# Performance work log

Hardware: AMD Instinct MI355X
Metric: run time of the kernel (lower is better)

The kernel has to match this reference:

```python
import jax, jax.numpy as jnp
import numpy as np

B, D, K, A = 32768, 256, 1024, 32
MIN_LOG_STD, MAX_LOG_STD = -20.0, 2.0


def setup_inputs() -> dict:
    key = jax.random.key(0)
    ks = jax.random.split(key, 9)
    return {
        "obs": jax.random.normal(ks[0], (B, D), dtype=jnp.float32),
        "mean_C": jax.random.normal(ks[1], (K, D), dtype=jnp.float32),
        "mean_sigma": jnp.abs(jax.random.normal(ks[2], (K,), dtype=jnp.float32)) + 0.1,
        "mean_w": jax.random.normal(ks[3], (A, K), dtype=jnp.float32),
        "mean_b": jax.random.normal(ks[4], (A,), dtype=jnp.float32),
        "std_C": jax.random.normal(ks[5], (K, D), dtype=jnp.float32),
        "std_sigma": jnp.abs(jax.random.normal(ks[6], (K,), dtype=jnp.float32)) + 0.1,
        "std_w": jax.random.normal(ks[7], (A, K), dtype=jnp.float32),
        "std_b": jax.random.normal(ks[8], (A,), dtype=jnp.float32),
    }


def _rbf(x, C, sigma_sq, w, b):
    # r[b,k] = sum_d (x[b,d] - C[k,d])^2, expanded to avoid a [B,K,D] intermediate
    x2 = jnp.sum(x * x, axis=-1, keepdims=True)           # [B,1]
    c2 = jnp.sum(C * C, axis=-1)[None, :]                  # [1,K]
    r = x2 - 2.0 * (x @ C.T) + c2                          # [B,K]
    phi = jnp.exp(-r / (2.0 * jnp.abs(sigma_sq)[None, :]))  # [B,K]
    return phi @ w.T + b[None, :]                          # [B,A]


def reference(obs, mean_C, mean_sigma, mean_w, mean_b,
              std_C, std_sigma, std_w, std_b):
    action_mean = _rbf(obs, mean_C, mean_sigma, mean_w, mean_b)
    std_raw = _rbf(obs, std_C, std_sigma, std_w, std_b)
    action_std = jnp.exp(jnp.clip(std_raw, MIN_LOG_STD, MAX_LOG_STD))
    return jnp.concatenate((action_mean, action_std), axis=-1)  # [B, 2A]
```

## Files before the change

kernel.cpp:

```cpp
#include <hip/hip_runtime.h>


typedef float floatx4 __attribute__((ext_vector_type(4)));
typedef int   intx4  __attribute__((ext_vector_type(4)));
typedef unsigned int u32;
typedef unsigned char u8;

constexpr float LOG2E = 1.4426950408889634f;
constexpr float QS    = 25.4f;
constexpr float SINV2 = (5.0f / 127.0f) * (5.0f / 127.0f);

__device__ __forceinline__ u32 pk_fp8(float a, float b, float c, float d) {
  u32 v = __builtin_amdgcn_cvt_pk_fp8_f32(a, b, 0u, 0);
  v = __builtin_amdgcn_cvt_pk_fp8_f32(c, d, v, 1);
  return v;
}
__device__ __forceinline__ long mk64(u32 lo, u32 hi) {
  return (long)lo | ((long)hi << 32);
}
__device__ __forceinline__ int q8(float x) {
  return (int)rintf(fminf(fmaxf(x * QS, -127.f), 127.f));
}
__device__ __forceinline__ u32 pk_i8(int a, int b, int c, int d) {
  return (u32)(a & 255) | ((u32)(b & 255) << 8) | ((u32)(c & 255) << 16) | ((u32)(d & 255) << 24);
}

__global__ void prep(const float* __restrict__ mC, const float* __restrict__ mS,
                     const float* __restrict__ sC, const float* __restrict__ sS,
                     const float* __restrict__ mw, const float* __restrict__ sw,
                     u8* __restrict__ Cb2, float* __restrict__ a2g,
                     float* __restrict__ g2n, u8* __restrict__ wt)
{
  const int blk = blockIdx.x;
  if (blk < 512) {
    const int wq = threadIdx.x >> 6;
    const int t  = threadIdx.x & 63;
    const int b  = blk * 4 + wq;
    const int half = b >> 10;
    const int k = b & 1023;
    const float* src = (half ? sC : mC) + (size_t)k * 256;
    float4 f = *(const float4*)(src + t * 4);
    int i0 = q8(f.x), i1 = q8(f.y), i2 = q8(f.z), i3 = q8(f.w);
    const int ct = b >> 6, row = b & 63;
    const int wvv = row >> 4, cc = row & 15;
    const int ks = t >> 4, qq = (t >> 2) & 3, j0 = (t & 3) * 4;
    *(u32*)(Cb2 + (size_t)ct * 16384 + wvv * 4096 + (ks * 64 + qq * 16 + cc) * 16 + j0) =
        pk_i8(i0, i1, i2, i3);
    int is = i0 * i0 + i1 * i1 + i2 * i2 + i3 * i3;
    for (int off = 32; off > 0; off >>= 1) is += __shfl_down(is, off, 64);
    if (t == 0) {
      float sig = fabsf((half ? sS : mS)[k]);
      float t2 = SINV2 * LOG2E * 0.5f / sig;
      a2g[b] = 2.f * t2;
      g2n[b] = -t2 * (float)is;
    }
  } else {
    const int m   = blk - 512;
    const int tid = threadIdx.x;
    const int wv  = tid >> 6;
    const int lane = tid & 63;
    const int c   = lane & 15;
    const int q   = lane >> 4;
    const int kbE = ((2 * m) & 15) * 64 + 16 * wv + 4 * q;
    const float* src = (m < 8) ? mw : sw;
    float4 f00 = *(const float4*)(src + (size_t)c * 1024 + kbE);
    float4 f01 = *(const float4*)(src + (size_t)c * 1024 + kbE + 64);
    float4 f10 = *(const float4*)(src + (size_t)(16 + c) * 1024 + kbE);
    float4 f11 = *(const float4*)(src + (size_t)(16 + c) * 1024 + kbE + 64);
    uint4 o;
    o.x = pk_fp8(f00.x, f00.y, f00.z, f00.w);
    o.y = pk_fp8(f01.x, f01.y, f01.z, f01.w);
    o.z = pk_fp8(f10.x, f10.y, f10.z, f10.w);
    o.w = pk_fp8(f11.x, f11.y, f11.z, f11.w);
    *(uint4*)(wt + ((size_t)m * 256 + tid) * 16) = o;
  }
}

__global__ __launch_bounds__(256, 4)
void policy_main(const float* __restrict__ obs,
                 const u8* __restrict__ Cb2,
                 const float* __restrict__ a2g,
                 const float* __restrict__ g2n,
                 const u8* __restrict__ wt,
                 const float* __restrict__ mbias,
                 const float* __restrict__ sbias,
                 float* __restrict__ out)
{
  __shared__ __align__(16) char smem[18432];
  float* x2p = (float*)(smem + 8192);
  float* red = (float*)smem;

  const int tid  = threadIdx.x;
  const int lane = tid & 63;
  const int wv   = tid >> 6;
  const int c    = lane & 15;
  const int q    = lane >> 4;
  const int half = blockIdx.x & 1;
  const int row0 = (blockIdx.x >> 1) * 32;
  const int kslc = 16 * wv + 4 * q;
  const int cfo  = wv * 4096 + lane * 16;

  const u8*    cbh = Cb2 + (size_t)half * (16 * 16384);
  const float* a2h = a2g + half * 1024;
  const float* g2h = g2n + half * 1024;
  const u8*    wtl = wt + (size_t)half * 32768 + (size_t)tid * 16;

#define LOADCF(CF, t)                                                     \
  { const u8* g0_ = cbh + (size_t)(t) * 16384 + cfo;                      \
    CF[0] = *(const intx4*)(g0_);                                         \
    CF[1] = *(const intx4*)(g0_ + 1024);                                  \
    CF[2] = *(const intx4*)(g0_ + 2048);                                  \
    CF[3] = *(const intx4*)(g0_ + 3072); }

  intx4 cfU[4], cfV[4];
  LOADCF(cfU, 0)
  LOADCF(cfV, 1)

  #pragma unroll
  for (int i = 0; i < 2; ++i) {
    int s = i * 256 + tid;
    int row = s >> 4;
    int s16 = s & 15;
    int l16 = s16 ^ (row & 15);
    const float* src = obs + (size_t)(row0 + row) * 256 + l16 * 16;
    float4 f0 = ((const float4*)src)[0];
    float4 f1 = ((const float4*)src)[1];
    float4 f2 = ((const float4*)src)[2];
    float4 f3 = ((const float4*)src)[3];
    int a0 = q8(f0.x), a1v = q8(f0.y), a2v = q8(f0.z), a3 = q8(f0.w);
    int b0 = q8(f1.x), b1 = q8(f1.y), b2 = q8(f1.z), b3 = q8(f1.w);
    int c0 = q8(f2.x), c1 = q8(f2.y), c2 = q8(f2.z), c3 = q8(f2.w);
    int d0 = q8(f3.x), d1 = q8(f3.y), d2 = q8(f3.z), d3 = q8(f3.w);
    uint4 pk;
    pk.x = pk_i8(a0, a1v, a2v, a3);
    pk.y = pk_i8(b0, b1, b2, b3);
    pk.z = pk_i8(c0, c1, c2, c3);
    pk.w = pk_i8(d0, d1, d2, d3);
    *(uint4*)(smem + s * 16) = pk;
    int is = a0*a0 + a1v*a1v + a2v*a2v + a3*a3
           + b0*b0 + b1*b1 + b2*b2 + b3*b3
           + c0*c0 + c1*c1 + c2*c2 + c3*c3
           + d0*d0 + d1*d1 + d2*d2 + d3*d3;
    x2p[row * 16 + s16] = (float)is;
  }
  __syncthreads();

  intx4 ob[2][4];
  #pragma unroll
  for (int nt = 0; nt < 2; ++nt) {
    const int row = nt * 16 + c;
    #pragma unroll
    for (int ks = 0; ks < 4; ++ks) {
      int slot = (4 * ks + q) ^ (row & 15);
      ob[nt][ks] = *(const intx4*)(smem + row * 256 + slot * 16);
    }
  }
  if (tid < 32) {
    float ssum = 0.f;
    #pragma unroll
    for (int j = 0; j < 16; j += 4) {
      float4 a = *(const float4*)(x2p + tid * 16 + j);
      ssum += a.x + a.y + a.z + a.w;
    }
    x2p[512 + tid] = ssum;
  }
  __syncthreads();

  float hx2[2];
  hx2[0] = 0.5f * x2p[512 + c];
  hx2[1] = 0.5f * x2p[512 + 16 + c];

  const intx4 Z4i = {0, 0, 0, 0};
  const floatx4 Z4 = {0.f, 0.f, 0.f, 0.f};
  floatx4 acc[2][2];
  #pragma unroll
  for (int a2i = 0; a2i < 2; ++a2i)
    #pragma unroll
    for (int nt = 0; nt < 2; ++nt) acc[a2i][nt] = Z4;

  intx4 a1E[2], a1O[2];
  u32 pE[2], pc[2];

#define GEMM1PAIR()                                                             \
  { _Pragma("unroll")                                                           \
    for (int nt = 0; nt < 2; ++nt) {                                            \
      a1E[nt] = __builtin_amdgcn_mfma_i32_16x16x64_i8(cfU[0], ob[nt][0], Z4i, 0, 0, 0); \
      a1O[nt] = __builtin_amdgcn_mfma_i32_16x16x64_i8(cfV[0], ob[nt][0], Z4i, 0, 0, 0); \
    }                                                                           \
    _Pragma("unroll")                                                           \
    for (int ks = 1; ks < 4; ++ks) {                                            \
      _Pragma("unroll")                                                         \
      for (int nt = 0; nt < 2; ++nt) {                                          \
        a1E[nt] = __builtin_amdgcn_mfma_i32_16x16x64_i8(cfU[ks], ob[nt][ks], a1E[nt], 0, 0, 0); \
        a1O[nt] = __builtin_amdgcn_mfma_i32_16x16x64_i8(cfV[ks], ob[nt][ks], a1O[nt], 0, 0, 0); \
      }                                                                         \
    } }

#define EXPP(A1, AC, GC, DST)                                                   \
  { _Pragma("unroll")                                                           \
    for (int nt = 0; nt < 2; ++nt) {                                            \
      float t0 = (float)A1[nt][0] - hx2[nt], t1 = (float)A1[nt][1] - hx2[nt];   \
      float t2 = (float)A1[nt][2] - hx2[nt], t3 = (float)A1[nt][3] - hx2[nt];   \
      DST[nt] = pk_fp8(__builtin_amdgcn_exp2f(fmaf(AC.x, t0, GC.x)),            \
                       __builtin_amdgcn_exp2f(fmaf(AC.y, t1, GC.y)),            \
                       __builtin_amdgcn_exp2f(fmaf(AC.z, t2, GC.z)),            \
                       __builtin_amdgcn_exp2f(fmaf(AC.w, t3, GC.w))); } }

#define GEMM2P(WV4)                                                             \
  { long wA0 = mk64(WV4.x, WV4.y), wA1 = mk64(WV4.z, WV4.w);                    \
    _Pragma("unroll")                                                           \
    for (int nt = 0; nt < 2; ++nt) {                                            \
      long pb = mk64(pE[nt], pc[nt]);                                           \
      acc[0][nt] = __builtin_amdgcn_mfma_f32_16x16x32_fp8_fp8(wA0, pb, acc[0][nt], 0, 0, 0); \
      acc[1][nt] = __builtin_amdgcn_mfma_f32_16x16x32_fp8_fp8(wA1, pb, acc[1][nt], 0, 0, 0); \
    } }

#define STEP(mm, PF)                                                            \
  {                                                                             \
    uint4 wv4 = *(const uint4*)(wtl + (size_t)(mm) * 4096);                     \
    float4 acE = *(const float4*)(a2h + (2 * (mm)) * 64 + kslc);                \
    float4 gcE = *(const float4*)(g2h + (2 * (mm)) * 64 + kslc);                \
    float4 acO = *(const float4*)(a2h + (2 * (mm) + 1) * 64 + kslc);            \
    float4 gcO = *(const float4*)(g2h + (2 * (mm) + 1) * 64 + kslc);            \
    GEMM1PAIR()                                                                 \
    if (PF) { LOADCF(cfU, 2 * (mm) + 2) LOADCF(cfV, 2 * (mm) + 3) }             \
    EXPP(a1E, acE, gcE, pE)                                                     \
    EXPP(a1O, acO, gcO, pc)                                                     \
    GEMM2P(wv4)                                                                 \
  }

  #pragma unroll
  for (int mm = 0; mm < 7; ++mm) STEP(mm, 1)
  STEP(7, 0)
#undef STEP
#undef GEMM1PAIR
#undef EXPP
#undef GEMM2P
#undef LOADCF

  __syncthreads();
  {
    float* myr = red + wv * 1152;
    #pragma unroll
    for (int a2i = 0; a2i < 2; ++a2i)
      #pragma unroll
      for (int nt = 0; nt < 2; ++nt)
        *(floatx4*)(myr + (nt * 16 + c) * 36 + a2i * 16 + 4 * q) = acc[a2i][nt];
  }
  __syncthreads();

  const float* bias = half ? sbias : mbias;
  #pragma unroll
  for (int i = 0; i < 4; ++i) {
    int idx = tid + 256 * i;
    int a = idx & 31;
    int b = idx >> 5;
    float v = red[b * 36 + a] + red[1152 + b * 36 + a] +
              red[2304 + b * 36 + a] + red[3456 + b * 36 + a];
    v += bias[a];
    if (half) {
      v = fminf(fmaxf(v, -20.f), 2.f);
      v = __builtin_amdgcn_exp2f(v * LOG2E);
    }
    out[(size_t)(row0 + b) * 64 + half * 32 + a] = v;
  }
}

extern "C" void kernel_launch(void* const* d_in, const int* in_sizes, int n_in,
                              void* d_out, int out_size, void* d_ws, size_t ws_size,
                              hipStream_t stream) {
  const float* obs = (const float*)d_in[0];
  const float* mC  = (const float*)d_in[1];
  const float* mS  = (const float*)d_in[2];
  const float* mW  = (const float*)d_in[3];
  const float* mB  = (const float*)d_in[4];
  const float* sC  = (const float*)d_in[5];
  const float* sS  = (const float*)d_in[6];
  const float* sW  = (const float*)d_in[7];
  const float* sB  = (const float*)d_in[8];
  float* out = (float*)d_out;

  u8*    Cb2 = (u8*)d_ws;
  float* a2g = (float*)((char*)d_ws + 2048 * 256);
  float* g2n = a2g + 2048;
  u8*    wt  = (u8*)(g2n + 2048);

  prep<<<528, 256, 0, stream>>>(mC, mS, sC, sS, mW, sW, Cb2, a2g, g2n, wt);
  policy_main<<<2048, 256, 0, stream>>>(obs, Cb2, a2g, g2n, wt, mB, sB, out);
}
```

Baseline: 119.6 us.

## Pre-quantize observations once in prep kernel into MFMA-ready int8 layout

Moves obs int8 quantization and squared-norm computation out of the main kernel into extra prep blocks. They write an MFMA-fragment-ordered int8 buffer and per-row half-norms to workspace. Previously both halves (mean and std) quantized the same rows. The main kernel now loads fragments directly from global memory, dropping the LDS staging and two barriers. This trades a global write and re-read of the int8 buffer for no longer reading fp32 obs twice.

```diff
diff --git a/kernel.cpp b/kernel.cpp
--- a/kernel.cpp
+++ b/kernel.cpp
@@ -28,8 +28,10 @@
 __global__ void prep(const float* __restrict__ mC, const float* __restrict__ mS,
                      const float* __restrict__ sC, const float* __restrict__ sS,
                      const float* __restrict__ mw, const float* __restrict__ sw,
+                     const float* __restrict__ obs,
                      u8* __restrict__ Cb2, float* __restrict__ a2g,
-                     float* __restrict__ g2n, u8* __restrict__ wt)
+                     float* __restrict__ g2n, u8* __restrict__ wt,
+                     u8* __restrict__ qb, float* __restrict__ hx2f)
 {
   const int blk = blockIdx.x;
   if (blk < 512) {
@@ -54,7 +56,7 @@
       a2g[b] = 2.f * t2;
       g2n[b] = -t2 * (float)is;
     }
-  } else {
+  } else if (blk < 528) {
     const int m   = blk - 512;
     const int tid = threadIdx.x;
     const int wv  = tid >> 6;
@@ -73,11 +75,25 @@
     o.z = pk_fp8(f10.x, f10.y, f10.z, f10.w);
     o.w = pk_fp8(f11.x, f11.y, f11.z, f11.w);
     *(uint4*)(wt + ((size_t)m * 256 + tid) * 16) = o;
+  } else {
+    const int wq = threadIdx.x >> 6;
+    const int t  = threadIdx.x & 63;
+    const int row = (blk - 528) * 4 + wq;
+    float4 f = *(const float4*)(obs + (size_t)row * 256 + t * 4);
+    int i0 = q8(f.x), i1 = q8(f.y), i2 = q8(f.z), i3 = q8(f.w);
+    const int T = row >> 4, c = row & 15;
+    const int ks = t >> 4, q = (t >> 2) & 3, j0 = (t & 3) * 4;
+    *(u32*)(qb + (size_t)T * 4096 + ks * 1024 + q * 256 + c * 16 + j0) =
+        pk_i8(i0, i1, i2, i3);
+    int is = i0 * i0 + i1 * i1 + i2 * i2 + i3 * i3;
+    for (int off = 32; off > 0; off >>= 1) is += __shfl_down(is, off, 64);
+    if (t == 0) hx2f[row] = 0.5f * (float)is;
   }
 }
 
 __global__ __launch_bounds__(256, 4)
-void policy_main(const float* __restrict__ obs,
+void policy_main(const u8* __restrict__ qb,
+                 const float* __restrict__ hx2f,
                  const u8* __restrict__ Cb2,
                  const float* __restrict__ a2g,
                  const float* __restrict__ g2n,
@@ -86,9 +102,7 @@
                  const float* __restrict__ sbias,
                  float* __restrict__ out)
 {
-  __shared__ __align__(16) char smem[18432];
-  float* x2p = (float*)(smem + 8192);
-  float* red = (float*)smem;
+  __shared__ __align__(16) float red[4608];
 
   const int tid  = threadIdx.x;
   const int lane = tid & 63;
@@ -116,59 +130,19 @@
   LOADCF(cfU, 0)
   LOADCF(cfV, 1)
 
-  #pragma unroll
-  for (int i = 0; i < 2; ++i) {
-    int s = i * 256 + tid;
-    int row = s >> 4;
-    int s16 = s & 15;
-    int l16 = s16 ^ (row & 15);
-    const float* src = obs + (size_t)(row0 + row) * 256 + l16 * 16;
-    float4 f0 = ((const float4*)src)[0];
-    float4 f1 = ((const float4*)src)[1];
-    float4 f2 = ((const float4*)src)[2];
-    float4 f3 = ((const float4*)src)[3];
-    int a0 = q8(f0.x), a1v = q8(f0.y), a2v = q8(f0.z), a3 = q8(f0.w);
-    int b0 = q8(f1.x), b1 = q8(f1.y), b2 = q8(f1.z), b3 = q8(f1.w);
-    int c0 = q8(f2.x), c1 = q8(f2.y), c2 = q8(f2.z), c3 = q8(f2.w);
-    int d0 = q8(f3.x), d1 = q8(f3.y), d2 = q8(f3.z), d3 = q8(f3.w);
-    uint4 pk;
-    pk.x = pk_i8(a0, a1v, a2v, a3);
-    pk.y = pk_i8(b0, b1, b2, b3);
-    pk.z = pk_i8(c0, c1, c2, c3);
-    pk.w = pk_i8(d0, d1, d2, d3);
-    *(uint4*)(smem + s * 16) = pk;
-    int is = a0*a0 + a1v*a1v + a2v*a2v + a3*a3
-           + b0*b0 + b1*b1 + b2*b2 + b3*b3
-           + c0*c0 + c1*c1 + c2*c2 + c3*c3
-           + d0*d0 + d1*d1 + d2*d2 + d3*d3;
-    x2p[row * 16 + s16] = (float)is;
-  }
-  __syncthreads();
-
   intx4 ob[2][4];
-  #pragma unroll
-  for (int nt = 0; nt < 2; ++nt) {
-    const int row = nt * 16 + c;
+  {
+    const u8* qrow = qb + (size_t)(row0 >> 4) * 4096 + lane * 16;
     #pragma unroll
-    for (int ks = 0; ks < 4; ++ks) {
-      int slot = (4 * ks + q) ^ (row & 15);
-      ob[nt][ks] = *(const intx4*)(smem + row * 256 + slot * 16);
-    }
-  }
-  if (tid < 32) {
-    float ssum = 0.f;
-    #pragma unroll
-    for (int j = 0; j < 16; j += 4) {
-      float4 a = *(const float4*)(x2p + tid * 16 + j);
-      ssum += a.x + a.y + a.z + a.w;
-    }
-    x2p[512 + tid] = ssum;
-  }
-  __syncthreads();
+    for (int nt = 0; nt < 2; ++nt)
+      #pragma unroll
+      for (int ks = 0; ks < 4; ++ks)
+        ob[nt][ks] = *(const intx4*)(qrow + nt * 4096 + ks * 1024);
+  }
 
   float hx2[2];
-  hx2[0] = 0.5f * x2p[512 + c];
-  hx2[1] = 0.5f * x2p[512 + 16 + c];
+  hx2[0] = hx2f[row0 + c];
+  hx2[1] = hx2f[row0 + 16 + c];
 
   const intx4 Z4i = {0, 0, 0, 0};
   const floatx4 Z4 = {0.f, 0.f, 0.f, 0.f};
@@ -238,7 +212,6 @@
 #undef GEMM2P
 #undef LOADCF
 
-  __syncthreads();
   {
     float* myr = red + wv * 1152;
     #pragma unroll
@@ -280,11 +253,13 @@
   const float* sB  = (const float*)d_in[8];
   float* out = (float*)d_out;
 
-  u8*    Cb2 = (u8*)d_ws;
-  float* a2g = (float*)((char*)d_ws + 2048 * 256);
-  float* g2n = a2g + 2048;
-  u8*    wt  = (u8*)(g2n + 2048);
-
-  prep<<<528, 256, 0, stream>>>(mC, mS, sC, sS, mW, sW, Cb2, a2g, g2n, wt);
-  policy_main<<<2048, 256, 0, stream>>>(obs, Cb2, a2g, g2n, wt, mB, sB, out);
-}
+  u8*    Cb2  = (u8*)d_ws;
+  float* a2g  = (float*)((char*)d_ws + 524288);
+  float* g2n  = a2g + 2048;
+  u8*    wt   = (u8*)(g2n + 2048);
+  u8*    qb   = (u8*)d_ws + 655360;
+  float* hx2f = (float*)((char*)d_ws + 655360 + 8388608);
+
+  prep<<<8720, 256, 0, stream>>>(mC, mS, sC, sS, mW, sW, obs, Cb2, a2g, g2n, wt, qb, hx2f);
+  policy_main<<<2048, 256, 0, stream>>>(qb, hx2f, Cb2, a2g, g2n, wt, mB, sB, out);
+}
```

Result: slower. 122.5 us (+2.4%).
